# Optimization experiments

Measured on AMD Instinct MI355X. Metric: run time of the kernel, lower is better.

## Reference

```python
import jax, jax.numpy as jnp
import numpy as np

N = 10000   # num nodes
E = 320000  # num edges (avg degree 32)
F = 128     # feat_size
H = 128     # hidden_size


def setup_inputs() -> dict:
    key = jax.random.key(0)
    ks = jax.random.split(key, 16)

    def p(k, shape, scale=0.05):
        return jax.random.normal(k, shape, jnp.float32) * scale

    inp = {
        "x": p(ks[0], (N, F), 1.0),
        "edge_index": jax.random.randint(ks[1], (2, E), 0, N),
    }
    # 6 SAGEConv layers: encoder (F->H, H->H), attr decoder (H->H, H->F),
    # struct decoder (H->H, H->N). Each has W_l (neighbor), b_l, W_r (root).
    dims = [(F, H), (H, H), (H, H), (H, F), (H, H), (H, N)]
    names = ["e1", "e2", "a1", "a2", "s1", "s2"]
    i = 2
    for name, (din, dout) in zip(names, dims):
        inp[f"Wl_{name}"] = p(ks[i], (din, dout))
        inp[f"bl_{name}"] = jnp.zeros((dout,), jnp.float32)
        inp[f"Wr_{name}"] = p(ks[i + 1], (din, dout))
        i += 2
    return inp


def sage(x, src, dst, Wl, bl, Wr, n):
    # PyG SAGEConv (aggr='mean'): mean of source-node features at each target,
    # then out = agg @ W_l + b + x @ W_r (root weight).
    msg = jax.ops.segment_sum(x[src], dst, num_segments=n)          # [n, din]
    deg = jax.ops.segment_sum(jnp.ones((src.shape[0],), x.dtype), dst, num_segments=n)
    agg = msg / jnp.maximum(deg, 1.0)[:, None]
    return agg @ Wl + bl + x @ Wr


def reference(x, edge_index,
              Wl_e1, bl_e1, Wr_e1, Wl_e2, bl_e2, Wr_e2,
              Wl_a1, bl_a1, Wr_a1, Wl_a2, bl_a2, Wr_a2,
              Wl_s1, bl_s1, Wr_s1, Wl_s2, bl_s2, Wr_s2):
    src, dst = edge_index[0], edge_index[1]
    n = x.shape[0]
    # Encoder (dropout is identity in eval mode)
    h = jax.nn.relu(sage(x, src, dst, Wl_e1, bl_e1, Wr_e1, n))
    h = jax.nn.relu(sage(h, src, dst, Wl_e2, bl_e2, Wr_e2, n))
    # Attribute decoder -> x_hat [N, F]
    xh = jax.nn.relu(sage(h, src, dst, Wl_a1, bl_a1, Wr_a1, n))
    xh = jax.nn.relu(sage(xh, src, dst, Wl_a2, bl_a2, Wr_a2, n))
    # Structure decoder -> [N, N], transposed as in the original
    s = jax.nn.relu(sage(h, src, dst, Wl_s1, bl_s1, Wr_s1, n))
    s = jax.nn.relu(sage(s, src, dst, Wl_s2, bl_s2, Wr_s2, n)).T
    return (s, xh)
```

## Files before the change

kernel.cpp:

```cpp
#include <hip/hip_runtime.h>
#include <hip/hip_bf16.h>

typedef unsigned short ushort_t;
typedef unsigned int uint_t;
typedef __attribute__((ext_vector_type(8))) short short8;
typedef __attribute__((ext_vector_type(4))) float float4v;

__device__ __forceinline__ float bf2f(ushort_t u) {
    union { uint_t i; float f; } c; c.i = ((uint_t)u) << 16; return c.f;
}
__device__ __forceinline__ ushort_t f2bf(float f) {
    union { float f; uint_t i; } c; c.f = f;
    uint_t x = c.i;
    uint_t r = x + 0x7fffu + ((x >> 16) & 1u);
    return (ushort_t)(r >> 16);
}

__device__ __forceinline__ void gl_lds16(const void* g, void* l) {
    __builtin_amdgcn_global_load_lds(
        (const __attribute__((address_space(1))) void*)g,
        (__attribute__((address_space(3))) void*)l, 16, 0, 0);
}

__device__ __forceinline__ void stv(float* p, float v) { *p = v; }
__device__ __forceinline__ void stv(ushort_t* p, float v) { *p = f2bf(v); }

__global__ void hist_kernel(const int* __restrict__ dstv, int* __restrict__ cnt, int E) {
    int e = blockIdx.x * 256 + threadIdx.x;
    if (e < E) atomicAdd(&cnt[dstv[e]], 1);
}

__global__ __launch_bounds__(1024) void scan_kernel(
    const int* __restrict__ cnt, int* __restrict__ rowptr,
    int* __restrict__ cursor, float* __restrict__ deginv, int n) {
    __shared__ int sums[1024];
    const int t = threadIdx.x;
    const int per = (n + 1023) >> 10;
    const int b0 = t * per;
    int s = 0;
    for (int u = 0; u < per; u++) {
        int i = b0 + u;
        if (i < n) s += cnt[i];
    }
    sums[t] = s;
    __syncthreads();
    int x = s;
    for (int off = 1; off < 1024; off <<= 1) {
        int y = (t >= off) ? sums[t - off] : 0;
        __syncthreads();
        x += y;
        sums[t] = x;
        __syncthreads();
    }
    int run = x - s;
    for (int u = 0; u < per; u++) {
        int i = b0 + u;
        if (i < n) {
            int v = cnt[i];
            rowptr[i] = run;
            cursor[i] = run;
            deginv[i] = 1.0f / (float)(v > 0 ? v : 1);
            run += v;
        }
    }
    if (t == 1023) rowptr[n] = x;
}

__global__ void scatter_kernel(const int* __restrict__ srcv, const int* __restrict__ dstv,
                               int* __restrict__ cursor, int* __restrict__ srcs_sorted, int E) {
    int e = blockIdx.x * 256 + threadIdx.x;
    if (e < E) {
        int p = atomicAdd(&cursor[dstv[e]], 1);
        srcs_sorted[p] = srcv[e];
    }
}

__global__ __launch_bounds__(256) void transpose_w_kernel(
    const float* __restrict__ W0, const float* __restrict__ W1,
    ushort_t* __restrict__ WT, int Nout) {
    __shared__ ushort_t tile[64][72];
    const int i0 = blockIdx.x * 64;
    const int k0 = blockIdx.y * 64;
    const float* W = (k0 < 128) ? (W0 + (size_t)k0 * Nout)
                                : (W1 + (size_t)(k0 - 128) * Nout);
    const int tid = threadIdx.x;
    const int li = tid & 63;
    const int kq = tid >> 6;
    const int gi = i0 + li;
    const bool ok = gi < Nout;
    for (int k = kq; k < 64; k += 4) {
        float v = ok ? W[(size_t)k * Nout + gi] : 0.f;
        tile[li][k] = f2bf(v);
    }
    __syncthreads();
    for (int s = tid; s < 512; s += 256) {
        int r = s >> 3, ch = s & 7;
        int gi2 = i0 + r;
        if (gi2 < Nout)
            *(short8*)(WT + (size_t)gi2 * 256 + k0 + ch * 8) = *(const short8*)&tile[r][ch * 8];
    }
}

struct W5 { const float* W0[5]; const float* W1[5]; };
__global__ __launch_bounds__(256) void transpose_w5_kernel(W5 wp, ushort_t* __restrict__ WT) {
    __shared__ ushort_t tile[64][72];
    const int layer = blockIdx.z;
    const int i0 = blockIdx.x * 64;
    const int k0 = blockIdx.y * 64;
    const float* W = (k0 < 128) ? (wp.W0[layer] + (size_t)k0 * 128)
                                : (wp.W1[layer] + (size_t)(k0 - 128) * 128);
    ushort_t* WTb = WT + (size_t)layer * 128 * 256;
    const int tid = threadIdx.x;
    const int li = tid & 63;
    const int kq = tid >> 6;
    const int gi = i0 + li;
    for (int k = kq; k < 64; k += 4)
        tile[li][k] = f2bf(W[(size_t)k * 128 + gi]);
    __syncthreads();
    for (int s = tid; s < 512; s += 256) {
        int r = s >> 3, ch = s & 7;
        *(short8*)(WTb + (size_t)(i0 + r) * 256 + k0 + ch * 8) = *(const short8*)&tile[r][ch * 8];
    }
}

template <typename TIN>
__device__ __forceinline__ float2 ld2(const TIN* act, size_t row, int t);
template <>
__device__ __forceinline__ float2 ld2<float>(const float* act, size_t row, int t) {
    return ((const float2*)act)[row * 64 + t];
}
template <>
__device__ __forceinline__ float2 ld2<ushort_t>(const ushort_t* act, size_t row, int t) {
    uint_t u = ((const uint_t*)act)[row * 64 + t];
    float2 r; r.x = bf2f((ushort_t)(u & 0xffffu)); r.y = bf2f((ushort_t)(u >> 16));
    return r;
}

template <typename TIN>
__global__ __launch_bounds__(256) void aggregate_kernel(
    const TIN* __restrict__ act, const int* __restrict__ srcs,
    const int* __restrict__ rowptr, const float* __restrict__ deginv,
    ushort_t* __restrict__ Acat, int N) {
    int node = blockIdx.x * 4 + (threadIdx.x >> 6);
    if (node >= N) return;
    int t = threadIdx.x & 63;
    int e0 = rowptr[node], e1 = rowptr[node + 1];
    float ax = 0.f, ay = 0.f;
    int e = e0;
    for (; e + 4 <= e1; e += 4) {
        int s0 = srcs[e], s1 = srcs[e + 1], s2 = srcs[e + 2], s3 = srcs[e + 3];
        float2 v0 = ld2(act, (size_t)s0, t);
        float2 v1 = ld2(act, (size_t)s1, t);
        float2 v2 = ld2(act, (size_t)s2, t);
        float2 v3 = ld2(act, (size_t)s3, t);
        ax += v0.x + v1.x + v2.x + v3.x;
        ay += v0.y + v1.y + v2.y + v3.y;
    }
    for (; e < e1; e++) {
        float2 v = ld2(act, (size_t)srcs[e], t);
        ax += v.x; ay += v.y;
    }
    float dinv = deginv[node];
    uint_t m = ((uint_t)f2bf(ay * dinv) << 16) | (uint_t)f2bf(ax * dinv);
    float2 self = ld2(act, (size_t)node, t);
    uint_t sf = ((uint_t)f2bf(self.y) << 16) | (uint_t)f2bf(self.x);
    ((uint_t*)Acat)[(size_t)node * 128 + t]      = m;
    ((uint_t*)Acat)[(size_t)node * 128 + 64 + t] = sf;
}

__global__ __launch_bounds__(256) void aggregate2_kernel(
    const ushort_t* __restrict__ act, const int* __restrict__ srcs,
    const int* __restrict__ rowptr, const float* __restrict__ deginv,
    ushort_t* __restrict__ AcatA, ushort_t* __restrict__ AcatS, int N) {
    int node = blockIdx.x * 4 + (threadIdx.x >> 6);
    if (node >= N) return;
    int t = threadIdx.x & 63;
    const uint_t* A = (const uint_t*)act;
    int e0 = rowptr[node], e1 = rowptr[node + 1];
    float ax = 0.f, ay = 0.f, sx = 0.f, sy = 0.f;
    int e = e0;
    for (; e + 4 <= e1; e += 4) {
        size_t r0 = (size_t)srcs[e] * 128,     r1 = (size_t)srcs[e + 1] * 128;
        size_t r2 = (size_t)srcs[e + 2] * 128, r3 = (size_t)srcs[e + 3] * 128;
        uint_t ua0 = A[r0 + t], us0 = A[r0 + 64 + t];
        uint_t ua1 = A[r1 + t], us1 = A[r1 + 64 + t];
        uint_t ua2 = A[r2 + t], us2 = A[r2 + 64 + t];
        uint_t ua3 = A[r3 + t], us3 = A[r3 + 64 + t];
        ax += bf2f((ushort_t)(ua0 & 0xffffu)) + bf2f((ushort_t)(ua1 & 0xffffu))
            + bf2f((ushort_t)(ua2 & 0xffffu)) + bf2f((ushort_t)(ua3 & 0xffffu));
        ay += bf2f((ushort_t)(ua0 >> 16))     + bf2f((ushort_t)(ua1 >> 16))
            + bf2f((ushort_t)(ua2 >> 16))     + bf2f((ushort_t)(ua3 >> 16));
        sx += bf2f((ushort_t)(us0 & 0xffffu)) + bf2f((ushort_t)(us1 & 0xffffu))
            + bf2f((ushort_t)(us2 & 0xffffu)) + bf2f((ushort_t)(us3 & 0xffffu));
        sy += bf2f((ushort_t)(us0 >> 16))     + bf2f((ushort_t)(us1 >> 16))
            + bf2f((ushort_t)(us2 >> 16))     + bf2f((ushort_t)(us3 >> 16));
    }
    for (; e < e1; e++) {
        size_t r0 = (size_t)srcs[e] * 128;
        uint_t ua0 = A[r0 + t], us0 = A[r0 + 64 + t];
        ax += bf2f((ushort_t)(ua0 & 0xffffu));
        ay += bf2f((ushort_t)(ua0 >> 16));
        sx += bf2f((ushort_t)(us0 & 0xffffu));
        sy += bf2f((ushort_t)(us0 >> 16));
    }
    float dinv = deginv[node];
    size_t rb = (size_t)node * 128;
    uint_t sa = A[rb + t], ss = A[rb + 64 + t];
    ((uint_t*)AcatA)[rb + t]      = ((uint_t)f2bf(ay * dinv) << 16) | (uint_t)f2bf(ax * dinv);
    ((uint_t*)AcatA)[rb + 64 + t] = sa;
    ((uint_t*)AcatS)[rb + t]      = ((uint_t)f2bf(sy * dinv) << 16) | (uint_t)f2bf(sx * dinv);
    ((uint_t*)AcatS)[rb + 64 + t] = ss;
}

template <bool BIAS_I, bool SWZ, int TM, typename TOUT>
__global__ __launch_bounds__(256) void gemm_nt_kernel(
    const ushort_t* __restrict__ A, const ushort_t* __restrict__ B,
    const float* __restrict__ bias, const float* __restrict__ bias2, int jsplit,
    TOUT* __restrict__ C, int rowsA, int rowsB, int tilesM, int tilesN) {
    constexpr int IMN = TM / 32;
    __shared__ __align__(16) char smem[TM * 128 + 16384];
    ushort_t* Alds = (ushort_t*)smem;
    ushort_t* Blds = (ushort_t*)(smem + TM * 128);

    int pid_m, pid_n;
    if (SWZ) {
        const int lin = blockIdx.x;
        const int nwg = gridDim.x;
        const int w = (lin & 7) * (nwg >> 3) + (lin >> 3);
        const int tM8 = (tilesM + 7) >> 3;
        const int sg = w >> 6, is = w & 63;
        const int sgm = sg % tM8, sgn = sg / tM8;
        pid_m = sgm * 8 + (is & 7);
        pid_n = sgn * 8 + (is >> 3);
        if (pid_m >= tilesM || pid_n >= tilesN) return;
    } else {
        const int lin = blockIdx.x;
        const int GRP = 8;
        const int nig = GRP * tilesN;
        const int gidg = lin / nig;
        const int first_m = gidg * GRP;
        const int gsz = min(tilesM - first_m, GRP);
        const int in_grp = lin - gidg * nig;
        pid_m = first_m + (in_grp % gsz);
        pid_n = in_grp / gsz;
    }
    const int i0 = pid_m * TM;
    const int j0 = pid_n * 128;

    const int tid  = threadIdx.x;
    const int lane = tid & 63;
    const int wid  = tid >> 6;
    const int wm = wid >> 1, wn = wid & 1;
    const int r16 = lane & 15, quad = lane >> 4;
    const int rsub = lane >> 3;
    const int csw  = (lane & 7) ^ rsub;

    float4v acc[IMN][4];
#pragma unroll
    for (int a = 0; a < IMN; a++)
#pragma unroll
        for (int b = 0; b < 4; b++) acc[a][b] = (float4v){0.f, 0.f, 0.f, 0.f};

    for (int kt = 0; kt < 4; kt++) {
        __syncthreads();
        const int kbase = kt * 64 + csw * 8;
#pragma unroll
        for (int t = 0; t < IMN; t++) {
            const int w8 = (wid * IMN + t) * 8;
            int rA = min(i0 + w8 + rsub, rowsA - 1);
            gl_lds16(A + (size_t)rA * 256 + kbase, Alds + w8 * 64);
        }
#pragma unroll
        for (int t = 0; t < 4; t++) {
            const int w8 = (wid * 4 + t) * 8;
            int rB = min(j0 + w8 + rsub, rowsB - 1);
            gl_lds16(B + (size_t)rB * 256 + kbase, Blds + w8 * 64);
        }
        __syncthreads();
#pragma unroll
        for (int ks = 0; ks < 2; ks++) {
            const int chb = ks * 4 + quad;
            const int sw = ((chb ^ (r16 & 7))) * 8;
            short8 af[IMN], bfr[4];
#pragma unroll
            for (int im = 0; im < IMN; im++)
                af[im] = *(const short8*)(Alds + (wm * (TM / 2) + im * 16 + r16) * 64 + sw);
#pragma unroll
            for (int jn = 0; jn < 4; jn++)
                bfr[jn] = *(const short8*)(Blds + (wn * 64 + jn * 16 + r16) * 64 + sw);
#pragma unroll
            for (int im = 0; im < IMN; im++)
#pragma unroll
                for (int jn = 0; jn < 4; jn++)
                    acc[im][jn] = __builtin_amdgcn_mfma_f32_16x16x32_bf16(
                        af[im], bfr[jn], acc[im][jn], 0, 0, 0);
        }
    }

    const int rows_lim = rowsA - i0;
    const int cols_lim = rowsB - j0;

    if constexpr (sizeof(TOUT) == 4) {
        float* T = (float*)smem;
        constexpr int NCH = TM / 32;
#pragma unroll
        for (int c = 0; c < NCH; c++) {
            const int crow = c * 32;
            __syncthreads();
            if (wm == crow / (TM / 2)) {
                const int imb = (crow - wm * (TM / 2)) / 16;
#pragma unroll
                for (int ii = 0; ii < 2; ii++) {
                    const int im = imb + ii;
#pragma unroll
                    for (int jn = 0; jn < 4; jn++) {
                        const int jl = wn * 64 + jn * 16 + r16;
                        float bj = 0.f;
                        if (!BIAS_I) {
                            int jg = j0 + jl;
                            bj = (jg >= jsplit) ? bias2[jg - jsplit] : bias[jg];
                        }
#pragma unroll
                        for (int r = 0; r < 4; r++) {
                            const int rl = ii * 16 + quad * 4 + r;
                            float bv = BIAS_I ? bias[min(i0 + crow + rl, rowsA - 1)] : bj;
                            T[rl * 132 + jl] = fmaxf(acc[im][jn][r] + bv, 0.f);
                        }
                    }
                }
            }
            __syncthreads();
            const int c4 = tid & 31, rl0 = tid >> 5;
#pragma unroll
            for (int s = 0; s < 4; s++) {
                const int rl = rl0 + s * 8;
                const int il = crow + rl;
                if (il < rows_lim) {
                    const int jl = c4 * 4;
                    float* dst = (float*)C + (size_t)(i0 + il) * rowsB + j0 + jl;
                    if (jl + 4 <= cols_lim) {
                        *(float4v*)dst = *(const float4v*)&T[rl * 132 + jl];
                    } else {
                        for (int jj = 0; jj < 4; jj++)
                            if (jl + jj < cols_lim) dst[jj] = T[rl * 132 + jl + jj];
                    }
                }
            }
        }
    } else {
#pragma unroll
        for (int im = 0; im < IMN; im++) {
#pragma unroll
            for (int jn = 0; jn < 4; jn++) {
                const int jl = wn * 64 + jn * 16 + r16;
                if (jl < cols_lim) {
                    float bj = 0.f;
                    if (!BIAS_I) {
                        int jg = j0 + jl;
                        bj = (jg >= jsplit) ? bias2[jg - jsplit] : bias[jg];
                    }
#pragma unroll
                    for (int r = 0; r < 4; r++) {
                        const int il = wm * (TM / 2) + im * 16 + quad * 4 + r;
                        if (il < rows_lim) {
                            float bv = BIAS_I ? bias[i0 + il] : bj;
                            float v = fmaxf(acc[im][jn][r] + bv, 0.f);
                            stv(C + (size_t)(i0 + il) * rowsB + (j0 + jl), v);
                        }
                    }
                }
            }
        }
    }
}

extern "C" void kernel_launch(void* const* d_in, const int* in_sizes, int n_in,
                              void* d_out, int out_size, void* d_ws, size_t ws_size,
                              hipStream_t stream) {
    const int N = in_sizes[18];
    const int E = in_sizes[1] / 2;

    const float* x = (const float*)d_in[0];
    const int* ei = (const int*)d_in[1];
    const int* srcv = ei;
    const int* dstv = ei + E;

    const float* Wl[6] = {(const float*)d_in[2],  (const float*)d_in[5],
                          (const float*)d_in[8],  (const float*)d_in[11],
                          (const float*)d_in[14], (const float*)d_in[17]};
    const float* bl[6] = {(const float*)d_in[3],  (const float*)d_in[6],
                          (const float*)d_in[9],  (const float*)d_in[12],
                          (const float*)d_in[15], (const float*)d_in[18]};
    const float* Wr[6] = {(const float*)d_in[4],  (const float*)d_in[7],
                          (const float*)d_in[10], (const float*)d_in[13],
                          (const float*)d_in[16], (const float*)d_in[19]};

    char* p = (char*)d_ws;
    auto carve = [&](size_t bytes) -> char* {
        char* q = p;
        p += (bytes + 255) & ~(size_t)255;
        return q;
    };
    int*      cnt    = (int*)carve((size_t)N * 4);
    int*      rowptr = (int*)carve((size_t)(N + 1) * 4);
    int*      cursor = (int*)carve((size_t)N * 4);
    float*    deginv = (float*)carve((size_t)N * 4);
    int*      srcs   = (int*)carve((size_t)E * 4);
    ushort_t* Acat   = (ushort_t*)carve((size_t)N * 256 * 2);
    ushort_t* AcatS  = (ushort_t*)carve((size_t)N * 256 * 2);
    ushort_t* hbA    = (ushort_t*)carve((size_t)N * 128 * 2);
    ushort_t* hbB    = (ushort_t*)carve((size_t)N * 128 * 2);
    ushort_t* hbC    = (ushort_t*)carve((size_t)N * 256 * 2);
    ushort_t* WTs2   = (ushort_t*)carve((size_t)N * 256 * 2);
    ushort_t* WsT    = (ushort_t*)carve((size_t)5 * 128 * 256 * 2);

    hipMemsetAsync(cnt, 0, (size_t)N * 4, stream);
    hist_kernel<<<(E + 255) / 256, 256, 0, stream>>>(dstv, cnt, E);
    scan_kernel<<<1, 1024, 0, stream>>>(cnt, rowptr, cursor, deginv, N);
    scatter_kernel<<<(E + 255) / 256, 256, 0, stream>>>(srcv, dstv, cursor, srcs, E);

    W5 w5;
    w5.W0[0] = Wl[0]; w5.W1[0] = Wr[0];
    w5.W0[1] = Wl[1]; w5.W1[1] = Wr[1];
    w5.W0[2] = Wl[2]; w5.W1[2] = Wr[2];
    w5.W0[3] = Wl[4]; w5.W1[3] = Wr[4];
    w5.W0[4] = Wl[3]; w5.W1[4] = Wr[3];
    transpose_w5_kernel<<<dim3(2, 4, 5), 256, 0, stream>>>(w5, WsT);
    transpose_w_kernel<<<dim3((N + 63) / 64, 4), 256, 0, stream>>>(
        Wl[5], Wr[5], WTs2, N);

    float* outp = (float*)d_out;
    float* xh_out = outp + (size_t)N * N;

    const int tM128 = (N + 127) / 128;
    const int tM64  = (N + 63) / 64;
    const int BIG = 1 << 30;

    aggregate_kernel<float><<<(N + 3) / 4, 256, 0, stream>>>(x, srcs, rowptr, deginv, Acat, N);
    gemm_nt_kernel<false, false, 64, ushort_t><<<tM64, 256, 0, stream>>>(
        Acat, WsT + 0 * 128 * 256, bl[0], nullptr, BIG, hbA, N, 128, tM64, 1);
    aggregate_kernel<ushort_t><<<(N + 3) / 4, 256, 0, stream>>>(hbA, srcs, rowptr, deginv, Acat, N);
    gemm_nt_kernel<false, false, 64, ushort_t><<<tM64, 256, 0, stream>>>(
        Acat, WsT + 1 * 128 * 256, bl[1], nullptr, BIG, hbB, N, 128, tM64, 1);
    aggregate_kernel<ushort_t><<<(N + 3) / 4, 256, 0, stream>>>(hbB, srcs, rowptr, deginv, Acat, N);
    gemm_nt_kernel<false, false, 64, ushort_t><<<tM64 * 2, 256, 0, stream>>>(
        Acat, WsT + 2 * 128 * 256, bl[2], bl[4], 128, hbC, N, 256, tM64, 2);
    aggregate2_kernel<<<(N + 3) / 4, 256, 0, stream>>>(hbC, srcs, rowptr, deginv, Acat, AcatS, N);
    gemm_nt_kernel<false, false, 64, float><<<tM64, 256, 0, stream>>>(
        Acat, WsT + 4 * 128 * 256, bl[3], nullptr, BIG, xh_out, N, 128, tM64, 1);
    const int tM8 = (tM128 + 7) / 8;
    gemm_nt_kernel<true, true, 128, float><<<tM8 * tM8 * 64, 256, 0, stream>>>(
        WTs2, AcatS, bl[5], nullptr, BIG, outp, N, N, tM128, tM128);

    (void)n_in; (void)out_size; (void)ws_size;
}
```

Baseline: 673.9 us.

## Double-buffer LDS tiles in GEMM and use nontemporal stores for fp32 output

```diff
diff --git a/kernel.cpp b/kernel.cpp
--- a/kernel.cpp
+++ b/kernel.cpp
@@ -218,9 +218,10 @@
     const float* __restrict__ bias, const float* __restrict__ bias2, int jsplit,
     TOUT* __restrict__ C, int rowsA, int rowsB, int tilesM, int tilesN) {
     constexpr int IMN = TM / 32;
-    __shared__ __align__(16) char smem[TM * 128 + 16384];
-    ushort_t* Alds = (ushort_t*)smem;
-    ushort_t* Blds = (ushort_t*)(smem + TM * 128);
+    constexpr int NLD = IMN + 4;
+    constexpr int ABYTES = TM * 128;
+    constexpr int BBYTES = 128 * 128;
+    __shared__ __align__(16) char smem[2 * (ABYTES + BBYTES)];
 
     int pid_m, pid_n;
     if (SWZ) {
@@ -261,22 +262,37 @@
 #pragma unroll
         for (int b = 0; b < 4; b++) acc[a][b] = (float4v){0.f, 0.f, 0.f, 0.f};
 
-    for (int kt = 0; kt < 4; kt++) {
-        __syncthreads();
+    auto stage = [&](int buf, int kt) {
+        ushort_t* Ad = (ushort_t*)(smem + buf * (ABYTES + BBYTES));
+        ushort_t* Bd = (ushort_t*)(smem + buf * (ABYTES + BBYTES) + ABYTES);
         const int kbase = kt * 64 + csw * 8;
 #pragma unroll
         for (int t = 0; t < IMN; t++) {
             const int w8 = (wid * IMN + t) * 8;
             int rA = min(i0 + w8 + rsub, rowsA - 1);
-            gl_lds16(A + (size_t)rA * 256 + kbase, Alds + w8 * 64);
+            gl_lds16(A + (size_t)rA * 256 + kbase, Ad + w8 * 64);
         }
 #pragma unroll
         for (int t = 0; t < 4; t++) {
             const int w8 = (wid * 4 + t) * 8;
             int rB = min(j0 + w8 + rsub, rowsB - 1);
-            gl_lds16(B + (size_t)rB * 256 + kbase, Blds + w8 * 64);
-        }
-        __syncthreads();
+            gl_lds16(B + (size_t)rB * 256 + kbase, Bd + w8 * 64);
+        }
+    };
+
+    stage(0, 0);
+#pragma unroll
+    for (int kt = 0; kt < 4; kt++) {
+        if (kt < 3) {
+            stage((kt + 1) & 1, kt + 1);
+            asm volatile("s_waitcnt vmcnt(%0)" :: "n"(NLD) : "memory");
+        } else {
+            asm volatile("s_waitcnt vmcnt(0)" ::: "memory");
+        }
+        __builtin_amdgcn_s_barrier();
+        asm volatile("" ::: "memory");
+        const ushort_t* Ac = (const ushort_t*)(smem + (kt & 1) * (ABYTES + BBYTES));
+        const ushort_t* Bc = Ac + ABYTES / 2;
 #pragma unroll
         for (int ks = 0; ks < 2; ks++) {
             const int chb = ks * 4 + quad;
@@ -284,16 +300,22 @@
             short8 af[IMN], bfr[4];
 #pragma unroll
             for (int im = 0; im < IMN; im++)
-                af[im] = *(const short8*)(Alds + (wm * (TM / 2) + im * 16 + r16) * 64 + sw);
+                af[im] = *(const short8*)(Ac + (wm * (TM / 2) + im * 16 + r16) * 64 + sw);
 #pragma unroll
             for (int jn = 0; jn < 4; jn++)
-                bfr[jn] = *(const short8*)(Blds + (wn * 64 + jn * 16 + r16) * 64 + sw);
+                bfr[jn] = *(const short8*)(Bc + (wn * 64 + jn * 16 + r16) * 64 + sw);
 #pragma unroll
             for (int im = 0; im < IMN; im++)
 #pragma unroll
                 for (int jn = 0; jn < 4; jn++)
                     acc[im][jn] = __builtin_amdgcn_mfma_f32_16x16x32_bf16(
                         af[im], bfr[jn], acc[im][jn], 0, 0, 0);
+        }
+        if (kt < 3) {
+            asm volatile("s_waitcnt lgkmcnt(0)" ::: "memory");
+            __builtin_amdgcn_sched_barrier(0);
+            __builtin_amdgcn_s_barrier();
+            asm volatile("" ::: "memory");
         }
     }
 
@@ -339,7 +361,8 @@
                     const int jl = c4 * 4;
                     float* dst = (float*)C + (size_t)(i0 + il) * rowsB + j0 + jl;
                     if (jl + 4 <= cols_lim) {
-                        *(float4v*)dst = *(const float4v*)&T[rl * 132 + jl];
+                        float4v vv = *(const float4v*)&T[rl * 132 + jl];
+                        __builtin_nontemporal_store(vv, (float4v*)dst);
                     } else {
                         for (int jj = 0; jj < 4; jj++)
                             if (jl + jj < cols_lim) dst[jj] = T[rl * 132 + jl + jj];
```

Measured after the change: 652.2 us. 1.03x faster.
